# Optimization experiments

Hardware: AMD Instinct MI355X
Metric: run time of the kernel (lower is better)

The kernel has to match this reference:

```python
import jax, jax.numpy as jnp
import numpy as np

N, T, H, D = 32, 2048, 1024, 384

def setup_inputs() -> dict:
    key = jax.random.key(0)
    k1, k2, k3, k4, k5 = jax.random.split(key, 5)
    scale_h = 1.0 / np.sqrt(H)
    scale_d = 1.0 / np.sqrt(D)
    return {
        "gru_output": jax.random.normal(k1, (N, T, H), dtype=jnp.float32),
        "condition": jax.random.normal(k2, (N, D), dtype=jnp.float32),
        "W_h": jax.random.normal(k3, (H, H), dtype=jnp.float32) * scale_h,
        "W_c": jax.random.normal(k4, (D, H), dtype=jnp.float32) * scale_d,
        "bias": jnp.zeros((H,), dtype=jnp.float32),
        "v": jax.random.normal(k5, (H,), dtype=jnp.float32) * scale_h,
    }

def reference(gru_output, condition, W_h, W_c, bias, v):
    # h_proj: (N, T, H); c_proj: (N, 1, H)
    h_proj = jnp.einsum("nth,hk->ntk", gru_output, W_h)
    c_proj = jnp.einsum("nd,dk->nk", condition, W_c)[:, None, :]
    energy = jnp.tanh(h_proj + c_proj + bias)          # (N, T, H)
    scores = jnp.einsum("ntk,k->nt", energy, v)        # (N, T)
    weights = jax.nn.softmax(scores, axis=-1)          # (N, T)
    context = jnp.einsum("nth,nt->nh", gru_output, weights)  # (N, H)
    return context
```

## Files before the change

### kernel.cpp

```cpp
#include <hip/hip_runtime.h>
#include <hip/hip_bf16.h>

#define N_B 32
#define T_S 2048
#define H_D 1024
#define D_C 384
#define NT  (N_B * T_S)

typedef __attribute__((ext_vector_type(8))) short bf16x8;
typedef __attribute__((ext_vector_type(4))) float f32x4;
typedef __attribute__((ext_vector_type(8))) unsigned short u16x8;

__device__ __forceinline__ ushort f2bf(float f) {
    union { float f; unsigned u; } x; x.f = f;
    unsigned u = x.u;
    unsigned r = (u + 0x7FFFu + ((u >> 16) & 1u)) >> 16;
    return (ushort)r;
}

__device__ __forceinline__ float bf2f(ushort u) {
    union { unsigned u; float f; } x; x.u = ((unsigned)u) << 16;
    return x.f;
}

__device__ __forceinline__ float fast_tanh(float x) {
    float e = __expf(2.0f * x);
    return 1.0f - 2.0f / (e + 1.0f);
}

__device__ __forceinline__ void gl2lds16(const void* g, void* l) {
    __builtin_amdgcn_global_load_lds(
        (const __attribute__((address_space(1))) void*)g,
        (__attribute__((address_space(3))) void*)l, 16, 0, 0);
}

__global__ __launch_bounds__(256) void convert_kernel(
    const float* __restrict__ g, ushort* __restrict__ gb)
{
    const size_t base = ((size_t)blockIdx.x * 256 + threadIdx.x) * 8;
    float4 v0 = *(const float4*)(g + base);
    float4 v1 = *(const float4*)(g + base + 4);
    u16x8 o;
    o[0] = f2bf(v0.x); o[1] = f2bf(v0.y); o[2] = f2bf(v0.z); o[3] = f2bf(v0.w);
    o[4] = f2bf(v1.x); o[5] = f2bf(v1.y); o[6] = f2bf(v1.z); o[7] = f2bf(v1.w);
    *(u16x8*)(gb + base) = o;
}

__global__ __launch_bounds__(256) void transpose_kernel(
    const float* __restrict__ W, ushort* __restrict__ Wt)
{
    __shared__ ushort tile[64 * 66];
    const int bx = blockIdx.x & 15;
    const int by = blockIdx.x >> 4;
    const int t = threadIdx.x;
    #pragma unroll
    for (int i = 0; i < 16; ++i) {
        int idx = t + i * 256;
        int r = idx >> 6, c = idx & 63;
        tile[r * 66 + c] = f2bf(W[(size_t)(by * 64 + r) * H_D + bx * 64 + c]);
    }
    __syncthreads();
    #pragma unroll
    for (int i = 0; i < 16; ++i) {
        int idx = t + i * 256;
        int r = idx >> 6, c = idx & 63;
        Wt[(size_t)(bx * 64 + r) * H_D + by * 64 + c] = tile[c * 66 + r];
    }
}

__global__ __launch_bounds__(256) void cproj_kernel(
    const float* __restrict__ cond, const float* __restrict__ Wc,
    const float* __restrict__ bias, float* __restrict__ cproj)
{
    const int idx = blockIdx.x * 256 + threadIdx.x;
    const int n = idx >> 10, k = idx & 1023;
    float a0 = bias[k], a1 = 0.f, a2 = 0.f, a3 = 0.f;
    const float* cp = cond + n * D_C;
    for (int d = 0; d < D_C; d += 4) {
        a0 = fmaf(cp[d + 0], Wc[(size_t)(d + 0) * H_D + k], a0);
        a1 = fmaf(cp[d + 1], Wc[(size_t)(d + 1) * H_D + k], a1);
        a2 = fmaf(cp[d + 2], Wc[(size_t)(d + 2) * H_D + k], a2);
        a3 = fmaf(cp[d + 3], Wc[(size_t)(d + 3) * H_D + k], a3);
    }
    cproj[idx] = (a0 + a1) + (a2 + a3);
}

__global__ __launch_bounds__(256) void gemm3_kernel(
    const ushort* __restrict__ Ab, const ushort* __restrict__ Wt,
    const float* __restrict__ cproj, const float* __restrict__ v,
    float* __restrict__ spart)
{
    __shared__ __align__(16) ushort As[128 * 64];
    __shared__ __align__(16) ushort Bs[128 * 64];
    __shared__ float red[2][2][4][16];
    const int id = blockIdx.x;
    const int mb = (id & 7) + ((id >> 6) << 3);
    const int kb = (id >> 3) & 7;
    const int m0 = mb * 128;
    const int nbatch = mb >> 4;
    const int t = threadIdx.x;
    const int lane = t & 63, wave = t >> 6;
    const int wm = wave & 1, wn = wave >> 1;
    const int q = lane >> 4, ln = lane & 15;
    const int x7 = ln & 7;

    const int srow = wave * 8 + (lane >> 3);
    const int koff = ((lane & 7) ^ (lane >> 3)) * 8;
    const ushort* ag = Ab + (size_t)(m0 + srow) * H_D + koff;
    const ushort* bg = Wt + (size_t)(kb * 128 + srow) * H_D + koff;

    f32x4 acc[4][4];
    #pragma unroll
    for (int i = 0; i < 4; ++i)
        #pragma unroll
        for (int j = 0; j < 4; ++j)
            acc[i][j] = (f32x4){0.f, 0.f, 0.f, 0.f};

    for (int h0 = 0; h0 < H_D; h0 += 64) {
        if (h0) __syncthreads();
        #pragma unroll
        for (int i = 0; i < 4; ++i) {
            gl2lds16(ag + h0 + i * 32 * H_D, As + i * 2048 + wave * 512);
            gl2lds16(bg + h0 + i * 32 * H_D, Bs + i * 2048 + wave * 512);
        }
        __syncthreads();
        #pragma unroll
        for (int kk = 0; kk < 2; ++kk) {
            bf16x8 a[4], b[4];
            #pragma unroll
            for (int i = 0; i < 4; ++i) {
                int row = wm * 64 + i * 16 + ln;
                a[i] = *(const bf16x8*)(&As[row * 64 + (((kk << 2) + q) ^ x7) * 8]);
            }
            #pragma unroll
            for (int j = 0; j < 4; ++j) {
                int row = wn * 64 + j * 16 + ln;
                b[j] = *(const bf16x8*)(&Bs[row * 64 + (((kk << 2) + q) ^ x7) * 8]);
            }
            #pragma unroll
            for (int i = 0; i < 4; ++i)
                #pragma unroll
                for (int j = 0; j < 4; ++j)
                    acc[i][j] = __builtin_amdgcn_mfma_f32_16x16x32_bf16(a[i], b[j], acc[i][j], 0, 0, 0);
        }
    }

    float cpv[4], vv[4];
    const float* cpn = cproj + nbatch * H_D;
    #pragma unroll
    for (int j = 0; j < 4; ++j) {
        int col = kb * 128 + wn * 64 + j * 16 + ln;
        cpv[j] = cpn[col];
        vv[j] = v[col];
    }
    #pragma unroll
    for (int i = 0; i < 4; ++i) {
        float s0 = 0.f, s1 = 0.f, s2 = 0.f, s3 = 0.f;
        #pragma unroll
        for (int j = 0; j < 4; ++j) {
            s0 += fast_tanh(acc[i][j][0] + cpv[j]) * vv[j];
            s1 += fast_tanh(acc[i][j][1] + cpv[j]) * vv[j];
            s2 += fast_tanh(acc[i][j][2] + cpv[j]) * vv[j];
            s3 += fast_tanh(acc[i][j][3] + cpv[j]) * vv[j];
        }
        #pragma unroll
        for (int off = 1; off < 16; off <<= 1) {
            s0 += __shfl_xor(s0, off);
            s1 += __shfl_xor(s1, off);
            s2 += __shfl_xor(s2, off);
            s3 += __shfl_xor(s3, off);
        }
        if (ln == 0) {
            red[wm][wn][i][q * 4 + 0] = s0;
            red[wm][wn][i][q * 4 + 1] = s1;
            red[wm][wn][i][q * 4 + 2] = s2;
            red[wm][wn][i][q * 4 + 3] = s3;
        }
    }
    __syncthreads();
    if (t < 128) {
        int wm2 = t >> 6, idx = t & 63;
        int i2 = idx >> 4, qr = idx & 15;
        float val = red[wm2][0][i2][qr] + red[wm2][1][i2][qr];
        spart[(size_t)kb * NT + m0 + wm2 * 64 + idx] = val;
    }
}

__global__ __launch_bounds__(256) void softmax8_kernel(
    const float* __restrict__ spart, float* __restrict__ weights)
{
    const int n = blockIdx.x;
    const int t = threadIdx.x;
    __shared__ float red[256];
    float sv[8];
    float m = -1e30f;
    #pragma unroll
    for (int i = 0; i < 8; ++i) {
        int mrow = n * T_S + i * 256 + t;
        float s = 0.f;
        #pragma unroll
        for (int kb = 0; kb < 8; ++kb) s += spart[(size_t)kb * NT + mrow];
        sv[i] = s;
        m = fmaxf(m, s);
    }
    red[t] = m; __syncthreads();
    for (int s = 128; s > 0; s >>= 1) {
        if (t < s) red[t] = fmaxf(red[t], red[t + s]);
        __syncthreads();
    }
    const float mx = red[0];
    __syncthreads();
    float sum = 0.f;
    #pragma unroll
    for (int i = 0; i < 8; ++i) { sv[i] = __expf(sv[i] - mx); sum += sv[i]; }
    red[t] = sum; __syncthreads();
    for (int s = 128; s > 0; s >>= 1) {
        if (t < s) red[t] += red[t + s];
        __syncthreads();
    }
    const float inv = 1.0f / red[0];
    #pragma unroll
    for (int i = 0; i < 8; ++i) weights[n * T_S + i * 256 + t] = sv[i] * inv;
}

__global__ __launch_bounds__(256) void context2_kernel(
    const ushort* __restrict__ Ab, const float* __restrict__ weights,
    float* __restrict__ out)
{
    const int tb = blockIdx.x;
    const int n  = blockIdx.y;
    const int t  = threadIdx.x;
    float a0 = 0.f, a1 = 0.f, a2 = 0.f, a3 = 0.f;
    const float* wp = weights + n * T_S + tb * 64;
    const ushort* gp = Ab + (size_t)(n * T_S + tb * 64) * H_D + t * 4;
    #pragma unroll 8
    for (int tt = 0; tt < 64; ++tt) {
        float w = wp[tt];
        ushort4 gv = *(const ushort4*)(gp + (size_t)tt * H_D);
        a0 = fmaf(w, bf2f(gv.x), a0);
        a1 = fmaf(w, bf2f(gv.y), a1);
        a2 = fmaf(w, bf2f(gv.z), a2);
        a3 = fmaf(w, bf2f(gv.w), a3);
    }
    float* op = out + n * H_D + t * 4;
    atomicAdd(op + 0, a0);
    atomicAdd(op + 1, a1);
    atomicAdd(op + 2, a2);
    atomicAdd(op + 3, a3);
}

extern "C" void kernel_launch(void* const* d_in, const int* in_sizes, int n_in,
                              void* d_out, int out_size, void* d_ws, size_t ws_size,
                              hipStream_t stream)
{
    const float* gru  = (const float*)d_in[0];
    const float* cond = (const float*)d_in[1];
    const float* W_h  = (const float*)d_in[2];
    const float* W_c  = (const float*)d_in[3];
    const float* bias = (const float*)d_in[4];
    const float* v    = (const float*)d_in[5];
    float* out = (float*)d_out;

    char* ws = (char*)d_ws;
    const size_t szAb    = (size_t)NT * H_D * 2;
    const size_t szWt    = (size_t)H_D * H_D * 2;
    const size_t szCproj = (size_t)N_B * H_D * 4;
    const size_t szSpart = (size_t)8 * NT * 4;

    ushort* Ab    = (ushort*)ws;
    ushort* Wt    = (ushort*)(ws + szAb);
    float* cproj  = (float*)(ws + szAb + szWt);
    float* spart  = (float*)(ws + szAb + szWt + szCproj);
    float* wts    = (float*)(ws + szAb + szWt + szCproj + szSpart);

    hipMemsetAsync(out, 0, N_B * H_D * sizeof(float), stream);
    convert_kernel<<<32768, 256, 0, stream>>>(gru, Ab);
    transpose_kernel<<<256, 256, 0, stream>>>(W_h, Wt);
    cproj_kernel<<<128, 256, 0, stream>>>(cond, W_c, bias, cproj);
    gemm3_kernel<<<4096, 256, 0, stream>>>(Ab, Wt, cproj, v, spart);
    softmax8_kernel<<<N_B, 256, 0, stream>>>(spart, wts);
    context2_kernel<<<dim3(32, N_B), 256, 0, stream>>>(Ab, wts, out);
}
```

Measured before the change: 581.2 us.

## Retune convert, split cproj over D, widen softmax, replace context atomics with reduction

The convert kernel now handles four elements per thread with twice the blocks. cproj is split four ways over the condition dimension and combined with atomics into a zeroed buffer. Softmax runs 1024 threads per row instead of 256. The context kernel writes per-tile partials, which a separate reduce kernel sums, replacing the atomics into the output. The reduction adds an extra launch, and the partials buffer reuses the spart workspace.

Measured after the change: 560.9 us. -3.5%, faster.

```diff
diff --git a/kernel.cpp b/kernel.cpp
--- a/kernel.cpp
+++ b/kernel.cpp
@@ -9,7 +9,6 @@
 
 typedef __attribute__((ext_vector_type(8))) short bf16x8;
 typedef __attribute__((ext_vector_type(4))) float f32x4;
-typedef __attribute__((ext_vector_type(8))) unsigned short u16x8;
 
 __device__ __forceinline__ ushort f2bf(float f) {
     union { float f; unsigned u; } x; x.f = f;
@@ -37,13 +36,11 @@
 __global__ __launch_bounds__(256) void convert_kernel(
     const float* __restrict__ g, ushort* __restrict__ gb)
 {
-    const size_t base = ((size_t)blockIdx.x * 256 + threadIdx.x) * 8;
-    float4 v0 = *(const float4*)(g + base);
-    float4 v1 = *(const float4*)(g + base + 4);
-    u16x8 o;
-    o[0] = f2bf(v0.x); o[1] = f2bf(v0.y); o[2] = f2bf(v0.z); o[3] = f2bf(v0.w);
-    o[4] = f2bf(v1.x); o[5] = f2bf(v1.y); o[6] = f2bf(v1.z); o[7] = f2bf(v1.w);
-    *(u16x8*)(gb + base) = o;
+    const size_t base = ((size_t)blockIdx.x * 256 + threadIdx.x) * 4;
+    float4 v = *(const float4*)(g + base);
+    ushort4 o;
+    o.x = f2bf(v.x); o.y = f2bf(v.y); o.z = f2bf(v.z); o.w = f2bf(v.w);
+    *(ushort4*)(gb + base) = o;
 }
 
 __global__ __launch_bounds__(256) void transpose_kernel(
@@ -74,15 +71,17 @@
 {
     const int idx = blockIdx.x * 256 + threadIdx.x;
     const int n = idx >> 10, k = idx & 1023;
-    float a0 = bias[k], a1 = 0.f, a2 = 0.f, a3 = 0.f;
+    const int d0 = blockIdx.y * 96;
+    float a0 = (blockIdx.y == 0) ? bias[k] : 0.f;
+    float a1 = 0.f, a2 = 0.f, a3 = 0.f;
     const float* cp = cond + n * D_C;
-    for (int d = 0; d < D_C; d += 4) {
+    for (int d = d0; d < d0 + 96; d += 4) {
         a0 = fmaf(cp[d + 0], Wc[(size_t)(d + 0) * H_D + k], a0);
         a1 = fmaf(cp[d + 1], Wc[(size_t)(d + 1) * H_D + k], a1);
         a2 = fmaf(cp[d + 2], Wc[(size_t)(d + 2) * H_D + k], a2);
         a3 = fmaf(cp[d + 3], Wc[(size_t)(d + 3) * H_D + k], a3);
     }
-    cproj[idx] = (a0 + a1) + (a2 + a3);
+    atomicAdd(&cproj[idx], (a0 + a1) + (a2 + a3));
 }
 
 __global__ __launch_bounds__(256) void gemm3_kernel(
@@ -186,55 +185,48 @@
     }
 }
 
-__global__ __launch_bounds__(256) void softmax8_kernel(
+__global__ __launch_bounds__(1024) void softmax8_kernel(
     const float* __restrict__ spart, float* __restrict__ weights)
 {
     const int n = blockIdx.x;
     const int t = threadIdx.x;
-    __shared__ float red[256];
-    float sv[8];
-    float m = -1e30f;
-    #pragma unroll
-    for (int i = 0; i < 8; ++i) {
-        int mrow = n * T_S + i * 256 + t;
-        float s = 0.f;
-        #pragma unroll
-        for (int kb = 0; kb < 8; ++kb) s += spart[(size_t)kb * NT + mrow];
-        sv[i] = s;
-        m = fmaxf(m, s);
-    }
-    red[t] = m; __syncthreads();
-    for (int s = 128; s > 0; s >>= 1) {
+    __shared__ float red[1024];
+    float s0 = 0.f, s1 = 0.f;
+    #pragma unroll
+    for (int kb = 0; kb < 8; ++kb) {
+        s0 += spart[(size_t)kb * NT + n * T_S + t];
+        s1 += spart[(size_t)kb * NT + n * T_S + 1024 + t];
+    }
+    red[t] = fmaxf(s0, s1); __syncthreads();
+    for (int s = 512; s > 0; s >>= 1) {
         if (t < s) red[t] = fmaxf(red[t], red[t + s]);
         __syncthreads();
     }
     const float mx = red[0];
     __syncthreads();
-    float sum = 0.f;
-    #pragma unroll
-    for (int i = 0; i < 8; ++i) { sv[i] = __expf(sv[i] - mx); sum += sv[i]; }
-    red[t] = sum; __syncthreads();
-    for (int s = 128; s > 0; s >>= 1) {
+    float e0 = __expf(s0 - mx), e1 = __expf(s1 - mx);
+    red[t] = e0 + e1; __syncthreads();
+    for (int s = 512; s > 0; s >>= 1) {
         if (t < s) red[t] += red[t + s];
         __syncthreads();
     }
     const float inv = 1.0f / red[0];
-    #pragma unroll
-    for (int i = 0; i < 8; ++i) weights[n * T_S + i * 256 + t] = sv[i] * inv;
-}
-
-__global__ __launch_bounds__(256) void context2_kernel(
+    weights[n * T_S + t] = e0 * inv;
+    weights[n * T_S + 1024 + t] = e1 * inv;
+}
+
+__global__ __launch_bounds__(256) void context3_kernel(
     const ushort* __restrict__ Ab, const float* __restrict__ weights,
-    float* __restrict__ out)
+    float* __restrict__ cpart)
 {
     const int tb = blockIdx.x;
     const int n  = blockIdx.y;
     const int t  = threadIdx.x;
     float a0 = 0.f, a1 = 0.f, a2 = 0.f, a3 = 0.f;
-    const float* wp = weights + n * T_S + tb * 64;
-    const ushort* gp = Ab + (size_t)(n * T_S + tb * 64) * H_D + t * 4;
+    const float* wp = weights + n * T_S + tb * 128;
+    const ushort* gp = Ab + (size_t)(n * T_S + tb * 128) * H_D + t * 4;
     #pragma unroll 8
-    for (int tt = 0; tt < 64; ++tt) {
+    for (int tt = 0; tt < 128; ++tt) {
         float w = wp[tt];
         ushort4 gv = *(const ushort4*)(gp + (size_t)tt * H_D);
         a0 = fmaf(w, bf2f(gv.x), a0);
@@ -242,11 +234,19 @@
         a2 = fmaf(w, bf2f(gv.z), a2);
         a3 = fmaf(w, bf2f(gv.w), a3);
     }
-    float* op = out + n * H_D + t * 4;
-    atomicAdd(op + 0, a0);
-    atomicAdd(op + 1, a1);
-    atomicAdd(op + 2, a2);
-    atomicAdd(op + 3, a3);
+    *(float4*)(cpart + ((size_t)tb * N_B + n) * H_D + t * 4) =
+        make_float4(a0, a1, a2, a3);
+}
+
+__global__ __launch_bounds__(256) void reduce_kernel(
+    const float* __restrict__ cpart, float* __restrict__ out)
+{
+    const int idx = blockIdx.x * 256 + threadIdx.x;
+    float s = 0.f;
+    #pragma unroll
+    for (int tb = 0; tb < 16; ++tb)
+        s += cpart[(size_t)tb * (N_B * H_D) + idx];
+    out[idx] = s;
 }
 
 extern "C" void kernel_launch(void* const* d_in, const int* in_sizes, int n_in,
@@ -271,13 +271,15 @@
     ushort* Wt    = (ushort*)(ws + szAb);
     float* cproj  = (float*)(ws + szAb + szWt);
     float* spart  = (float*)(ws + szAb + szWt + szCproj);
+    float* cpart  = spart;
     float* wts    = (float*)(ws + szAb + szWt + szCproj + szSpart);
 
-    hipMemsetAsync(out, 0, N_B * H_D * sizeof(float), stream);
-    convert_kernel<<<32768, 256, 0, stream>>>(gru, Ab);
+    hipMemsetAsync(cproj, 0, szCproj, stream);
+    convert_kernel<<<65536, 256, 0, stream>>>(gru, Ab);
     transpose_kernel<<<256, 256, 0, stream>>>(W_h, Wt);
-    cproj_kernel<<<128, 256, 0, stream>>>(cond, W_c, bias, cproj);
+    cproj_kernel<<<dim3(128, 4), 256, 0, stream>>>(cond, W_c, bias, cproj);
     gemm3_kernel<<<4096, 256, 0, stream>>>(Ab, Wt, cproj, v, spart);
-    softmax8_kernel<<<N_B, 256, 0, stream>>>(spart, wts);
-    context2_kernel<<<dim3(32, N_B), 256, 0, stream>>>(Ab, wts, out);
-}
+    softmax8_kernel<<<N_B, 1024, 0, stream>>>(spart, wts);
+    context3_kernel<<<dim3(16, N_B), 256, 0, stream>>>(Ab, wts, cpart);
+    reduce_kernel<<<128, 256, 0, stream>>>(cpart, out);
+}
```
